# Kernel tuning notes

Hardware: AMD Instinct MI355X
Metric: run time of the kernel (lower is better)

Reference implementation:

```python
import jax, jax.numpy as jnp
import numpy as np

L_LEVELS = 10
LEVEL_DIM = 4
BASE_RES = 16
T_HASH = 2 ** 21
DEG_VIEW = 4
DENSITY_BIAS = -1.0
RGB_PADDING = 0.001
RES = (BASE_RES * 2 ** np.arange(L_LEVELS)).astype(np.float32)  # 16..8192
CORNERS = np.array([[(i >> 2) & 1, (i >> 1) & 1, i & 1] for i in range(8)], np.int32)  # [8,3]
P1 = jnp.uint32(2654435761)
P2 = jnp.uint32(805459861)


def hash_grid_encode(pts, embeddings):
    """pts [N,3] in [-1,1]; embeddings [L,T,D] -> [N,L,D] trilinear hash-grid features."""
    x01 = (pts + 1.0) * 0.5  # [N,3] in [0,1]

    def level(emb, r):
        pos = x01 * r - 0.5  # align_corners=False style
        p0 = jnp.floor(pos)
        frac = pos - p0  # [N,3]
        coords = (p0.astype(jnp.int32)[:, None, :] + CORNERS).astype(jnp.uint32)  # [N,8,3]
        h = coords[..., 0] ^ (coords[..., 1] * P1) ^ (coords[..., 2] * P2)
        idx = (h & jnp.uint32(T_HASH - 1)).astype(jnp.int32)  # [N,8]
        w = jnp.prod(jnp.where(CORNERS == 1, frac[:, None, :], 1.0 - frac[:, None, :]), axis=-1)  # [N,8]
        vals = emb[idx]  # [N,8,D]
        return jnp.einsum('ncd,nc->nd', vals, w)

    feats = jax.vmap(level)(embeddings, jnp.asarray(RES))  # [L,N,D]
    return jnp.moveaxis(feats, 0, 1)  # [N,L,D]


def pos_enc(d, min_deg=0, max_deg=DEG_VIEW):
    scales = 2.0 ** jnp.arange(min_deg, max_deg, dtype=jnp.float32)
    xb = (d[..., None, :] * scales[:, None]).reshape(*d.shape[:-1], -1)  # [...,3*deg]
    four = jnp.sin(jnp.concatenate([xb, xb + 0.5 * jnp.pi], axis=-1))
    return jnp.concatenate([d, four], axis=-1)  # [..., 3 + 6*deg] = 27


def setup_inputs() -> dict:
    key = jax.random.key(0)
    ks = jax.random.split(key, 10)
    B, S, n = 1024, 32, 6
    means = jax.random.uniform(ks[0], (B, S, n, 3), minval=-1.0, maxval=1.0)
    stds = jax.random.uniform(ks[1], (B, S, n), minval=0.001, maxval=0.05)
    vd = jax.random.normal(ks[2], (B, 3))
    viewdirs = vd / jnp.linalg.norm(vd, axis=-1, keepdims=True)
    embeddings = jax.random.normal(ks[3], (L_LEVELS, T_HASH, LEVEL_DIM)) * 0.1

    def lin(k, i, o):
        return jax.random.normal(k, (i, o)) * (1.0 / np.sqrt(i))

    return {
        'rand': 0,
        'means': means, 'stds': stds, 'viewdirs': viewdirs, 'embeddings': embeddings,
        'Wd0': lin(ks[4], 40, 64), 'bd0': jnp.zeros(64),
        'Wd1': lin(ks[5], 64, 256), 'bd1': jnp.zeros(256),
        'Wv0': lin(ks[6], 283, 256), 'bv0': jnp.zeros(256),
        'Wv1': lin(ks[7], 539, 256), 'bv1': jnp.zeros(256),
        'Wr': lin(ks[8], 256, 3), 'br': jnp.zeros(3),
    }


def reference(rand, means, stds, viewdirs, embeddings, Wd0, bd0, Wd1, bd1,
              Wv0, bv0, Wv1, bv1, Wr, br):
    B, S, n = means.shape[:3]
    # --- predict_density ---
    feats = hash_grid_encode(means.reshape(-1, 3), embeddings)
    feats = feats.reshape(B, S, n, L_LEVELS, LEVEL_DIM)
    gs = jnp.asarray(RES)
    # erf re-weighting by per-level grid size (ZipNeRF anti-aliasing)
    w = jax.lax.erf(1.0 / jnp.clip(jnp.sqrt(8.0 * stds[..., None] ** 2 * gs ** 2), 1e-10))  # [B,S,n,L]
    feat = (feats * w[..., None]).mean(axis=-3).reshape(B, S, L_LEVELS * LEVEL_DIM)  # mean over multisamples n
    h = jax.nn.relu(feat @ Wd0 + bd0)
    x = h @ Wd1 + bd1  # [B,S,256] bottleneck
    density = jax.nn.softplus(x[..., 0] + DENSITY_BIAS)
    # --- view-dependent rgb branch ---
    dir_enc = pos_enc(viewdirs)  # [B,27]
    de = jnp.broadcast_to(dir_enc[:, None, :], (B, S, dir_enc.shape[-1]))
    x_in = jnp.concatenate([x, de], axis=-1)  # [B,S,283]
    h = jax.nn.relu(x_in @ Wv0 + bv0)
    h = jnp.concatenate([h, x_in], axis=-1)  # skip connection at layer 0 -> [B,S,539]
    h = jax.nn.relu(h @ Wv1 + bv1)
    rgb = jax.nn.sigmoid(h @ Wr + br)  # rgb_premultiplier=1, rgb_bias=0
    rgb = rgb * (1.0 + 2.0 * RGB_PADDING) - RGB_PADDING
    return density, rgb
```

## Files before the change

### kernel.cpp

```cpp
#include <hip/hip_runtime.h>

#define HASH_T    2097152u
#define HASH_MASK 2097151u
#define PRIME1 2654435761u
#define PRIME2 805459861u

typedef __attribute__((ext_vector_type(8))) short bf16x8;
typedef __attribute__((ext_vector_type(4))) float f32x4;
typedef __attribute__((ext_vector_type(4))) unsigned short us4;

#define LDS_STRIDE 328

__device__ __forceinline__ unsigned short bf16_hi(float x){
    unsigned u = __float_as_uint(x);
    return (unsigned short)((u + 0x7FFFu + ((u >> 16) & 1u)) >> 16);
}
__device__ __forceinline__ float bf16f(unsigned short h){
    return __uint_as_float((unsigned)h << 16);
}
__device__ __forceinline__ void split2(float x, unsigned short& h, unsigned short& l){
    h = bf16_hi(x);
    l = bf16_hi(x - bf16f(h));
}

__global__ __launch_bounds__(256) void pack_weights_kernel(
    const float* __restrict__ Wd0, const float* __restrict__ Wd1,
    const float* __restrict__ Wv0, const float* __restrict__ Wv1,
    unsigned short* __restrict__ pk)
{
    int tid = blockIdx.x * 256 + threadIdx.x;
    if (tid >= 424 * 512) return;
    int pair = tid >> 9;
    int li   = tid & 511;
    int lane = li >> 3, j = li & 7;
    int kq = ((lane >> 4) << 3) + j;
    int cl = lane & 15;
    float w;
    if (pair < 8) {
        int idx = pair; int kt = idx >> 2, ct = idx & 3;
        int k = kt * 32 + kq, c = ct * 16 + cl;
        w = (k < 40) ? Wd0[k * 64 + c] : 0.0f;
    } else if (pair < 40) {
        int idx = pair - 8; int kt = idx >> 4, ct = idx & 15;
        int k = kt * 32 + kq, c = ct * 16 + cl;
        w = Wd1[k * 256 + c];
    } else if (pair < 168) {
        int idx = pair - 40; int kt = idx >> 4, ct = idx & 15;
        int k = kt * 32 + kq, c = ct * 16 + cl;
        w = Wv0[k * 256 + c];
    } else {
        int idx = pair - 168;
        int kt = idx >> 4, ct = idx & 15;
        int k = kt * 32 + kq, c = ct * 16 + cl;
        int refr = (k < 256) ? (k + 256) : (k - 256);
        w = Wv1[refr * 256 + c];
    }
    unsigned short h, l; split2(w, h, l);
    pk[(size_t)pair * 1024 + li]       = h;
    pk[(size_t)pair * 1024 + 512 + li] = l;
}

__global__ __launch_bounds__(256) void hash_encode_kernel(
    const float* __restrict__ means, const float* __restrict__ stds,
    const float* __restrict__ emb, float* __restrict__ feat, int NS)
{
    int gid = blockIdx.x * 256 + threadIdx.x;
    if (gid >= NS * 10) return;
    int l = gid / NS;
    int s = gid - l * NS;
    float r = (float)(16 << l);
    const float* __restrict__ embL = emb + (size_t)l * (size_t)HASH_T * 4u;

    float a0 = 0.f, a1 = 0.f, a2 = 0.f, a3 = 0.f;
    #pragma unroll
    for (int n = 0; n < 6; ++n) {
        const float* mp = means + ((size_t)s * 6 + n) * 3;
        float sd = stds[(size_t)s * 6 + n];
        float px = (mp[0] + 1.0f) * 0.5f * r - 0.5f;
        float py = (mp[1] + 1.0f) * 0.5f * r - 0.5f;
        float pz = (mp[2] + 1.0f) * 0.5f * r - 0.5f;
        float fx = floorf(px), fy = floorf(py), fz = floorf(pz);
        float rx = px - fx, ry = py - fy, rz = pz - fz;
        int ix = (int)fx, iy = (int)fy, iz = (int)fz;
        unsigned hx[2] = { (unsigned)ix,          (unsigned)(ix + 1) };
        unsigned hy[2] = { (unsigned)iy * PRIME1, (unsigned)(iy + 1) * PRIME1 };
        unsigned hz[2] = { (unsigned)iz * PRIME2, (unsigned)(iz + 1) * PRIME2 };
        float wx[2] = { 1.0f - rx, rx };
        float wy[2] = { 1.0f - ry, ry };
        float wz[2] = { 1.0f - rz, rz };
        float t8 = 8.0f * (sd * sd) * (r * r);
        float wl = erff(1.0f / fmaxf(sqrtf(t8), 1e-10f));
        float v0 = 0.f, v1 = 0.f, v2 = 0.f, v3 = 0.f;
        #pragma unroll
        for (int c = 0; c < 8; ++c) {
            int bx = (c >> 2) & 1, by = (c >> 1) & 1, bz = c & 1;
            unsigned idx = (hx[bx] ^ hy[by] ^ hz[bz]) & HASH_MASK;
            const float4 e = *reinterpret_cast<const float4*>(embL + (size_t)idx * 4u);
            float w = wx[bx] * wy[by] * wz[bz];
            v0 += w * e.x; v1 += w * e.y; v2 += w * e.z; v3 += w * e.w;
        }
        a0 += wl * v0; a1 += wl * v1; a2 += wl * v2; a3 += wl * v3;
    }
    const float inv6 = 1.0f / 6.0f;
    float4 o; o.x = a0 * inv6; o.y = a1 * inv6; o.z = a2 * inv6; o.w = a3 * inv6;
    *reinterpret_cast<float4*>(feat + (size_t)s * 40 + l * 4) = o;
}

template<int KT, int NC>
__device__ __forceinline__ void gemm32(
    const unsigned short* __restrict__ pkBase, int NCT, int ct0, int kOff,
    const unsigned short (*Ahi)[LDS_STRIDE], const unsigned short (*Alo)[LDS_STRIDE],
    int lane, f32x4 acc[NC][2])
{
    const int r = lane & 15;
    const int kg = (lane >> 4) * 8;
    bf16x8 ah[NC], al[NC];
    #pragma unroll
    for (int ci = 0; ci < NC; ++ci) {
        const unsigned short* pf = pkBase + (size_t)(ct0 + ci) * 1024 + (size_t)lane * 8;
        ah[ci] = *reinterpret_cast<const bf16x8*>(pf);
        al[ci] = *reinterpret_cast<const bf16x8*>(pf + 512);
    }
    #pragma unroll
    for (int kt = 0; kt < KT; ++kt) {
        bf16x8 ahn[NC], aln[NC];
        if (kt + 1 < KT) {
            #pragma unroll
            for (int ci = 0; ci < NC; ++ci) {
                const unsigned short* pf = pkBase
                    + (size_t)((kt + 1) * NCT + ct0 + ci) * 1024 + (size_t)lane * 8;
                ahn[ci] = *reinterpret_cast<const bf16x8*>(pf);
                aln[ci] = *reinterpret_cast<const bf16x8*>(pf + 512);
            }
        }
        const int ke = kOff + kt * 32 + kg;
        bf16x8 bh[2], bl[2];
        #pragma unroll
        for (int st = 0; st < 2; ++st) {
            bh[st] = *reinterpret_cast<const bf16x8*>(&Ahi[st * 16 + r][ke]);
            bl[st] = *reinterpret_cast<const bf16x8*>(&Alo[st * 16 + r][ke]);
        }
        #pragma unroll
        for (int ci = 0; ci < NC; ++ci) {
            #pragma unroll
            for (int st = 0; st < 2; ++st) {
                acc[ci][st] = __builtin_amdgcn_mfma_f32_16x16x32_bf16(ah[ci], bh[st], acc[ci][st], 0, 0, 0);
                acc[ci][st] = __builtin_amdgcn_mfma_f32_16x16x32_bf16(ah[ci], bl[st], acc[ci][st], 0, 0, 0);
                acc[ci][st] = __builtin_amdgcn_mfma_f32_16x16x32_bf16(al[ci], bh[st], acc[ci][st], 0, 0, 0);
            }
        }
        if (kt + 1 < KT) {
            #pragma unroll
            for (int ci = 0; ci < NC; ++ci) { ah[ci] = ahn[ci]; al[ci] = aln[ci]; }
        }
    }
}

template<int NC, bool RELU>
__device__ __forceinline__ void epi32(
    f32x4 acc[NC][2], int ct0, int lane, const float* bias, int outOff,
    unsigned short (*Ahi)[LDS_STRIDE], unsigned short (*Alo)[LDS_STRIDE])
{
    const int r = lane & 15, g = lane >> 4;
    #pragma unroll
    for (int ci = 0; ci < NC; ++ci) {
        const int c0 = (ct0 + ci) * 16 + g * 4;
        const float4 bb = *reinterpret_cast<const float4*>(&bias[c0]);
        #pragma unroll
        for (int st = 0; st < 2; ++st) {
            const int s = st * 16 + r;
            float v[4] = { acc[ci][st][0] + bb.x, acc[ci][st][1] + bb.y,
                           acc[ci][st][2] + bb.z, acc[ci][st][3] + bb.w };
            us4 H, L;
            #pragma unroll
            for (int q = 0; q < 4; ++q) {
                float vv = RELU ? fmaxf(v[q], 0.0f) : v[q];
                unsigned short h, l; split2(vv, h, l);
                H[q] = h; L[q] = l;
            }
            *reinterpret_cast<us4*>(&Ahi[s][outOff + c0]) = H;
            *reinterpret_cast<us4*>(&Alo[s][outOff + c0]) = L;
        }
    }
}

__global__ __launch_bounds__(256, 3) void mlp_mfma_kernel(
    const float* __restrict__ feat, const float* __restrict__ vdirs,
    const unsigned short* __restrict__ pk,
    const float* __restrict__ bd0, const float* __restrict__ bd1,
    const float* __restrict__ Wv0, const float* __restrict__ bv0,
    const float* __restrict__ Wv1, const float* __restrict__ bv1,
    const float* __restrict__ Wr,  const float* __restrict__ br,
    float* __restrict__ outD, float* __restrict__ outRGB)
{
    __shared__ __align__(16) unsigned short sAhi[32][LDS_STRIDE];
    __shared__ __align__(16) unsigned short sAlo[32][LDS_STRIDE];
    __shared__ float sDe[32];
    __shared__ float sDv0[256];
    __shared__ float sDv1[256];

    const int t = threadIdx.x;
    const int lane = t & 63;
    const int w = t >> 6;
    const int b = blockIdx.x;
    const int base = b * 32;

    {
        int s = t >> 3, kg = t & 7;
        float v[8];
        if (kg < 5) {
            const float4 f0 = *reinterpret_cast<const float4*>(feat + (size_t)(base + s) * 40 + kg * 8);
            const float4 f1 = *reinterpret_cast<const float4*>(feat + (size_t)(base + s) * 40 + kg * 8 + 4);
            v[0]=f0.x; v[1]=f0.y; v[2]=f0.z; v[3]=f0.w;
            v[4]=f1.x; v[5]=f1.y; v[6]=f1.z; v[7]=f1.w;
        } else {
            #pragma unroll
            for (int q = 0; q < 8; ++q) v[q] = 0.0f;
        }
        us4 H0, H1, L0v, L1v;
        #pragma unroll
        for (int q = 0; q < 4; ++q) {
            unsigned short h, l;
            split2(v[q], h, l);       H0[q] = h; L0v[q] = l;
            split2(v[q + 4], h, l);   H1[q] = h; L1v[q] = l;
        }
        *reinterpret_cast<us4*>(&sAhi[s][kg * 8])     = H0;
        *reinterpret_cast<us4*>(&sAhi[s][kg * 8 + 4]) = H1;
        *reinterpret_cast<us4*>(&sAlo[s][kg * 8])     = L0v;
        *reinterpret_cast<us4*>(&sAlo[s][kg * 8 + 4]) = L1v;
    }
    if (t < 27) {
        float d0 = vdirs[b * 3 + 0], d1 = vdirs[b * 3 + 1], d2 = vdirs[b * 3 + 2];
        float val;
        if (t < 3) val = (t == 0) ? d0 : ((t == 1) ? d1 : d2);
        else {
            int u = t - 3, half = u / 12, jk = u % 12;
            int j = jk / 3, k = jk % 3;
            float dk = (k == 0) ? d0 : ((k == 1) ? d1 : d2);
            float xb = dk * (float)(1 << j);
            val = sinf(half ? (xb + 1.57079632679489662f) : xb);
        }
        sDe[t] = val;
    }
    __syncthreads();

    {
        int c = t;
        float a0 = bv0[c], a1 = bv1[c];
        #pragma unroll 3
        for (int k = 0; k < 27; ++k) {
            float dv = sDe[k];
            a0 += dv * Wv0[(256 + k) * 256 + c];
            a1 += dv * Wv1[(512 + k) * 256 + c];
        }
        sDv0[c] = a0; sDv1[c] = a1;
    }
    __syncthreads();

    {
        f32x4 acc[1][2] = {};
        gemm32<2, 1>(pk, 4, w, 0, sAhi, sAlo, lane, acc);
        __syncthreads();
        epi32<1, true>(acc, w, lane, bd0, 0, sAhi, sAlo);
    }
    __syncthreads();

    {
        f32x4 acc[4][2] = {};
        gemm32<2, 4>(pk + 8192, 16, w * 4, 0, sAhi, sAlo, lane, acc);
        if (w == 0 && (lane >> 4) == 0) {
            #pragma unroll
            for (int st = 0; st < 2; ++st) {
                float x0 = acc[0][st][0] + bd1[0];
                int s = st * 16 + (lane & 15);
                float vv = x0 - 1.0f;
                outD[base + s] = fmaxf(vv, 0.0f) + log1pf(expf(-fabsf(vv)));
            }
        }
        __syncthreads();
        epi32<4, false>(acc, w * 4, lane, bd1, 64, sAhi, sAlo);
    }
    __syncthreads();

    f32x4 px[4][2] = {};
    gemm32<8, 4>(pk + 172032, 16, w * 4, 64, sAhi, sAlo, lane, px);
    __syncthreads();

    {
        f32x4 acc[4][2] = {};
        gemm32<8, 4>(pk + 40960, 16, w * 4, 64, sAhi, sAlo, lane, acc);
        __syncthreads();
        epi32<4, true>(acc, w * 4, lane, sDv0, 64, sAhi, sAlo);
    }
    __syncthreads();

    {
        gemm32<8, 4>(pk + 303104, 16, w * 4, 64, sAhi, sAlo, lane, px);
        __syncthreads();
        epi32<4, true>(px, w * 4, lane, sDv1, 64, sAhi, sAlo);
    }
    __syncthreads();

    {
        int s = t >> 3, j = t & 7, k0 = 64 + j * 32;
        float p0 = 0.f, p1 = 0.f, p2 = 0.f;
        #pragma unroll 2
        for (int q = 0; q < 4; ++q) {
            us4 vh[2], vl[2];
            *reinterpret_cast<uint4*>(vh) = *reinterpret_cast<const uint4*>(&sAhi[s][k0 + q * 8]);
            *reinterpret_cast<uint4*>(vl) = *reinterpret_cast<const uint4*>(&sAlo[s][k0 + q * 8]);
            #pragma unroll
            for (int e = 0; e < 8; ++e) {
                int k = j * 32 + q * 8 + e;
                float hv = bf16f(((const unsigned short*)vh)[e]) + bf16f(((const unsigned short*)vl)[e]);
                p0 += hv * Wr[k * 3 + 0];
                p1 += hv * Wr[k * 3 + 1];
                p2 += hv * Wr[k * 3 + 2];
            }
        }
        #pragma unroll
        for (int m = 1; m < 8; m <<= 1) {
            p0 += __shfl_xor(p0, m);
            p1 += __shfl_xor(p1, m);
            p2 += __shfl_xor(p2, m);
        }
        if (j < 3) {
            float a = ((j == 0) ? p0 : (j == 1) ? p1 : p2) + br[j];
            float sg = 1.0f / (1.0f + expf(-a));
            outRGB[(size_t)(base + s) * 3 + j] = sg * 1.002f - 0.001f;
        }
    }
}

extern "C" void kernel_launch(void* const* d_in, const int* in_sizes, int n_in,
                              void* d_out, int out_size, void* d_ws, size_t ws_size,
                              hipStream_t stream) {
    const float* means = (const float*)d_in[1];
    const float* stds_ = (const float*)d_in[2];
    const float* vdirs = (const float*)d_in[3];
    const float* emb   = (const float*)d_in[4];
    const float* Wd0 = (const float*)d_in[5];
    const float* bd0 = (const float*)d_in[6];
    const float* Wd1 = (const float*)d_in[7];
    const float* bd1 = (const float*)d_in[8];
    const float* Wv0 = (const float*)d_in[9];
    const float* bv0 = (const float*)d_in[10];
    const float* Wv1 = (const float*)d_in[11];
    const float* bv1 = (const float*)d_in[12];
    const float* Wr  = (const float*)d_in[13];
    const float* br  = (const float*)d_in[14];

    const int B  = in_sizes[3] / 3;
    const int NS = B * 32;

    float* feat = (float*)d_ws;
    unsigned short* pk = (unsigned short*)((char*)d_ws + (size_t)NS * 40 * 4);

    hipLaunchKernelGGL(pack_weights_kernel, dim3((424 * 512 + 255) / 256), dim3(256), 0, stream,
                       Wd0, Wd1, Wv0, Wv1, pk);

    int total = NS * 10;
    hipLaunchKernelGGL(hash_encode_kernel, dim3((total + 255) / 256), dim3(256), 0, stream,
                       means, stds_, emb, feat, NS);

    float* outD   = (float*)d_out;
    float* outRGB = outD + NS;
    hipLaunchKernelGGL(mlp_mfma_kernel, dim3(B), dim3(256), 0, stream,
                       feat, vdirs, pk, bd0, bd1, Wv0, bv0, Wv1, bv1, Wr, br,
                       outD, outRGB);
}
```

Before: 224.0 us.

## Merge two same-input GEMMs into one dual pass and roll GEMM k-loops

```diff
diff --git a/kernel.cpp b/kernel.cpp
--- a/kernel.cpp
+++ b/kernel.cpp
@@ -107,32 +107,15 @@
 }
 
 template<int KT, int NC>
-__device__ __forceinline__ void gemm32(
+__device__ __forceinline__ void gemm32_rolled(
     const unsigned short* __restrict__ pkBase, int NCT, int ct0, int kOff,
     const unsigned short (*Ahi)[LDS_STRIDE], const unsigned short (*Alo)[LDS_STRIDE],
     int lane, f32x4 acc[NC][2])
 {
     const int r = lane & 15;
     const int kg = (lane >> 4) * 8;
-    bf16x8 ah[NC], al[NC];
-    #pragma unroll
-    for (int ci = 0; ci < NC; ++ci) {
-        const unsigned short* pf = pkBase + (size_t)(ct0 + ci) * 1024 + (size_t)lane * 8;
-        ah[ci] = *reinterpret_cast<const bf16x8*>(pf);
-        al[ci] = *reinterpret_cast<const bf16x8*>(pf + 512);
-    }
-    #pragma unroll
+    #pragma unroll 1
     for (int kt = 0; kt < KT; ++kt) {
-        bf16x8 ahn[NC], aln[NC];
-        if (kt + 1 < KT) {
-            #pragma unroll
-            for (int ci = 0; ci < NC; ++ci) {
-                const unsigned short* pf = pkBase
-                    + (size_t)((kt + 1) * NCT + ct0 + ci) * 1024 + (size_t)lane * 8;
-                ahn[ci] = *reinterpret_cast<const bf16x8*>(pf);
-                aln[ci] = *reinterpret_cast<const bf16x8*>(pf + 512);
-            }
-        }
         const int ke = kOff + kt * 32 + kg;
         bf16x8 bh[2], bl[2];
         #pragma unroll
@@ -142,16 +125,54 @@
         }
         #pragma unroll
         for (int ci = 0; ci < NC; ++ci) {
+            const unsigned short* pf = pkBase + (size_t)(kt * NCT + ct0 + ci) * 1024 + (size_t)lane * 8;
+            bf16x8 ah = *reinterpret_cast<const bf16x8*>(pf);
+            bf16x8 al = *reinterpret_cast<const bf16x8*>(pf + 512);
             #pragma unroll
             for (int st = 0; st < 2; ++st) {
-                acc[ci][st] = __builtin_amdgcn_mfma_f32_16x16x32_bf16(ah[ci], bh[st], acc[ci][st], 0, 0, 0);
-                acc[ci][st] = __builtin_amdgcn_mfma_f32_16x16x32_bf16(ah[ci], bl[st], acc[ci][st], 0, 0, 0);
-                acc[ci][st] = __builtin_amdgcn_mfma_f32_16x16x32_bf16(al[ci], bh[st], acc[ci][st], 0, 0, 0);
-            }
-        }
-        if (kt + 1 < KT) {
-            #pragma unroll
-            for (int ci = 0; ci < NC; ++ci) { ah[ci] = ahn[ci]; al[ci] = aln[ci]; }
+                acc[ci][st] = __builtin_amdgcn_mfma_f32_16x16x32_bf16(ah, bh[st], acc[ci][st], 0, 0, 0);
+                acc[ci][st] = __builtin_amdgcn_mfma_f32_16x16x32_bf16(ah, bl[st], acc[ci][st], 0, 0, 0);
+                acc[ci][st] = __builtin_amdgcn_mfma_f32_16x16x32_bf16(al, bh[st], acc[ci][st], 0, 0, 0);
+            }
+        }
+    }
+}
+
+__device__ __forceinline__ void gemm32_dual(
+    const unsigned short* __restrict__ pA, const unsigned short* __restrict__ pB,
+    int ct0, int kOff,
+    const unsigned short (*Ahi)[LDS_STRIDE], const unsigned short (*Alo)[LDS_STRIDE],
+    int lane, f32x4 accA[4][2], f32x4 accB[4][2])
+{
+    const int r = lane & 15;
+    const int kg = (lane >> 4) * 8;
+    #pragma unroll 1
+    for (int kt = 0; kt < 8; ++kt) {
+        const int ke = kOff + kt * 32 + kg;
+        bf16x8 bh[2], bl[2];
+        #pragma unroll
+        for (int st = 0; st < 2; ++st) {
+            bh[st] = *reinterpret_cast<const bf16x8*>(&Ahi[st * 16 + r][ke]);
+            bl[st] = *reinterpret_cast<const bf16x8*>(&Alo[st * 16 + r][ke]);
+        }
+        #pragma unroll
+        for (int ci = 0; ci < 4; ++ci) {
+            const size_t off = (size_t)(kt * 16 + ct0 + ci) * 1024 + (size_t)lane * 8;
+            const unsigned short* fA = pA + off;
+            bf16x8 ahA = *reinterpret_cast<const bf16x8*>(fA);
+            bf16x8 alA = *reinterpret_cast<const bf16x8*>(fA + 512);
+            const unsigned short* fB = pB + off;
+            bf16x8 ahB = *reinterpret_cast<const bf16x8*>(fB);
+            bf16x8 alB = *reinterpret_cast<const bf16x8*>(fB + 512);
+            #pragma unroll
+            for (int st = 0; st < 2; ++st) {
+                accA[ci][st] = __builtin_amdgcn_mfma_f32_16x16x32_bf16(ahA, bh[st], accA[ci][st], 0, 0, 0);
+                accA[ci][st] = __builtin_amdgcn_mfma_f32_16x16x32_bf16(ahA, bl[st], accA[ci][st], 0, 0, 0);
+                accA[ci][st] = __builtin_amdgcn_mfma_f32_16x16x32_bf16(alA, bh[st], accA[ci][st], 0, 0, 0);
+                accB[ci][st] = __builtin_amdgcn_mfma_f32_16x16x32_bf16(ahB, bh[st], accB[ci][st], 0, 0, 0);
+                accB[ci][st] = __builtin_amdgcn_mfma_f32_16x16x32_bf16(ahB, bl[st], accB[ci][st], 0, 0, 0);
+                accB[ci][st] = __builtin_amdgcn_mfma_f32_16x16x32_bf16(alB, bh[st], accB[ci][st], 0, 0, 0);
+            }
         }
     }
 }
@@ -259,7 +280,7 @@
 
     {
         f32x4 acc[1][2] = {};
-        gemm32<2, 1>(pk, 4, w, 0, sAhi, sAlo, lane, acc);
+        gemm32_rolled<2, 1>(pk, 4, w, 0, sAhi, sAlo, lane, acc);
         __syncthreads();
         epi32<1, true>(acc, w, lane, bd0, 0, sAhi, sAlo);
     }
@@ -267,7 +288,7 @@
 
     {
         f32x4 acc[4][2] = {};
-        gemm32<2, 4>(pk + 8192, 16, w * 4, 0, sAhi, sAlo, lane, acc);
+        gemm32_rolled<2, 4>(pk + 8192, 16, w * 4, 0, sAhi, sAlo, lane, acc);
         if (w == 0 && (lane >> 4) == 0) {
             #pragma unroll
             for (int st = 0; st < 2; ++st) {
@@ -283,19 +304,16 @@
     __syncthreads();
 
     f32x4 px[4][2] = {};
-    gemm32<8, 4>(pk + 172032, 16, w * 4, 64, sAhi, sAlo, lane, px);
-    __syncthreads();
-
     {
         f32x4 acc[4][2] = {};
-        gemm32<8, 4>(pk + 40960, 16, w * 4, 64, sAhi, sAlo, lane, acc);
+        gemm32_dual(pk + 172032, pk + 40960, w * 4, 64, sAhi, sAlo, lane, px, acc);
         __syncthreads();
         epi32<4, true>(acc, w * 4, lane, sDv0, 64, sAhi, sAlo);
     }
     __syncthreads();
 
     {
-        gemm32<8, 4>(pk + 303104, 16, w * 4, 64, sAhi, sAlo, lane, px);
+        gemm32_rolled<8, 4>(pk + 303104, 16, w * 4, 64, sAhi, sAlo, lane, px);
         __syncthreads();
         epi32<4, true>(px, w * 4, lane, sDv1, 64, sAhi, sAlo);
     }
@@ -304,7 +322,7 @@
     {
         int s = t >> 3, j = t & 7, k0 = 64 + j * 32;
         float p0 = 0.f, p1 = 0.f, p2 = 0.f;
-        #pragma unroll 2
+        #pragma unroll 1
         for (int q = 0; q < 4; ++q) {
             us4 vh[2], vl[2];
             *reinterpret_cast<uint4*>(vh) = *reinterpret_cast<const uint4*>(&sAhi[s][k0 + q * 8]);
```

Result: slower. 232.6 us (+3.8%).
